# Performance work log

Hardware: AMD Instinct MI355X
Metric: run time of the kernel (lower is better)

The kernel has to match this reference:

```python
import jax, jax.numpy as jnp
import numpy as np

OMEGA_ENC = 0.01   # Encoder.omega
OMEGA_K = 0.1      # KernelMLP.omega
N0, E0 = 4096, 16384     # level-0 graph
N1, E1 = 1024, 8192      # level-1 (pooled) graph
F_IN, H, LAT, DIM = 8, 64, 32, 3
F = H + DIM              # conv input features (x || pos)


def _glorot(key, shape):
    s = jnp.sqrt(2.0 / (shape[0] + shape[-1]))
    return (jax.random.normal(key, shape) * s).astype(jnp.float32)


def setup_inputs() -> dict:
    key = jax.random.key(0)
    ks = jax.random.split(key, 24)
    inp = {
        "x": jax.random.normal(ks[0], (N0, F_IN), jnp.float32),
        "pos": jax.random.normal(ks[1], (N0, DIM), jnp.float32),
        "edge_index": jax.random.randint(ks[2], (2, E0), 0, N0),
        "pool_edge_index1": jax.random.randint(ks[3], (2, E1), 0, N1),
        "pool_pos1": jax.random.normal(ks[4], (N1, DIM), jnp.float32),
        "pool_keep_idx0": jnp.sort(jax.random.randint(ks[5], (N1,), 0, N0)),
        "lin0_w": _glorot(ks[6], (F_IN, H)),
        "lin0_b": 0.01 * jax.random.normal(ks[7], (H,), jnp.float32),
        "lin1_w": _glorot(ks[8], (H, LAT)),
        "lin1_b": 0.01 * jax.random.normal(ks[9], (LAT,), jnp.float32),
    }
    k = 10
    for i in range(2):
        inp[f"conv{i}_k_w0"] = _glorot(ks[k], (DIM + 1, H))
        inp[f"conv{i}_k_b0"] = 0.01 * jax.random.normal(ks[k + 1], (H,), jnp.float32)
        inp[f"conv{i}_k_w1"] = _glorot(ks[k + 2], (H, H))
        inp[f"conv{i}_k_b1"] = 0.01 * jax.random.normal(ks[k + 3], (H,), jnp.float32)
        inp[f"conv{i}_k_w2"] = _glorot(ks[k + 4], (H, F))
        inp[f"conv{i}_k_b2"] = 0.01 * jax.random.normal(ks[k + 5], (F,), jnp.float32)
        inp[f"conv{i}_bias"] = jnp.zeros((H,), jnp.float32)  # zeros() init in torch
        k += 6
    return inp


def _with_self_loops(ei, n):
    # add_remaining_self_loops: input edges are assumed self-loop-free
    loops = jnp.arange(n, dtype=ei.dtype)
    return jnp.concatenate([ei, jnp.stack([loops, loops])], axis=1)


def _kernel_conv(xf, ei, pos, n, w0, b0, w1, b1, w2, b2, bias):
    src, dst = ei[0], ei[1]
    rel = pos[dst] - pos[src]                               # [E,3]
    zero = jnp.all(rel == 0.0, axis=1)                      # self loops -> rho=0, nan phi in torch
    rel_s = jnp.where(zero[:, None], 1.0, rel)              # safe values (avoid nan grads)
    rho = jnp.sqrt(jnp.sum(rel_s * rel_s, axis=1))
    theta = jnp.arctan2(rel_s[:, 1], rel_s[:, 0])
    phi = jnp.arcsin(jnp.clip(rel_s[:, 2] / rho, -1.0, 1.0))
    # torch sets theta/phi to 0 where phi is nan (rho==0); rho itself is 0 there
    rho = jnp.where(zero, 0.0, rho)
    theta = jnp.where(zero, 0.0, theta)
    phi = jnp.where(zero, 0.0, phi)
    feats = jnp.stack([rho, theta / jnp.pi, phi / jnp.pi], axis=1)   # [E,3]
    # KernelMLP lin0 on (feats || channel_id), evaluated for all out channels at once
    base = feats @ w0[:DIM] + b0                            # [E,H]
    ch = jnp.arange(H, dtype=xf.dtype)                      # out_channels == H
    h0 = jnp.sin(OMEGA_K * (base[None] + ch[:, None, None] * w0[DIM][None, None]))  # [C,E,H]
    h1 = jnp.sin(OMEGA_K * (jnp.einsum('ceh,hk->cek', h0, w1) + b1))                # [C,E,H]
    x_j = xf[src]                                           # [E,F]
    # msg[e,c] = (lin2(h1[c,e]) * x_j[e]).sum(); lin2 folded into the contraction
    msg = jnp.einsum('ceh,hf,ef->ec', h1, w2, x_j) + (x_j @ b2)[:, None]            # [E,C]
    return jax.ops.segment_sum(msg, dst, num_segments=n) + bias


def reference(x, edge_index, pos, pool_edge_index1, pool_pos1, pool_keep_idx0,
              lin0_w, lin0_b, lin1_w, lin1_b,
              conv0_k_w0, conv0_k_b0, conv0_k_w1, conv0_k_b1, conv0_k_w2, conv0_k_b2, conv0_bias,
              conv1_k_w0, conv1_k_b0, conv1_k_w1, conv1_k_b1, conv1_k_w2, conv1_k_b2, conv1_bias):
    n0 = x.shape[0]
    h = jnp.sin(OMEGA_ENC * (x @ lin0_w + lin0_b))
    ei0 = _with_self_loops(edge_index, n0)
    h = jnp.sin(OMEGA_ENC * _kernel_conv(jnp.concatenate([h, pos], 1), ei0, pos, n0,
                                         conv0_k_w0, conv0_k_b0, conv0_k_w1, conv0_k_b1,
                                         conv0_k_w2, conv0_k_b2, conv0_bias))
    # max_pool_neighbor_x: per-node max over neighbors incl. self (self loops in ei0)
    h = jax.ops.segment_max(h[ei0[0]], ei0[1], num_segments=n0)[pool_keep_idx0]
    n1 = pool_pos1.shape[0]
    ei1 = _with_self_loops(pool_edge_index1, n1)
    h = jnp.sin(OMEGA_ENC * _kernel_conv(jnp.concatenate([h, pool_pos1], 1), ei1, pool_pos1, n1,
                                         conv1_k_w0, conv1_k_b0, conv1_k_w1, conv1_k_b1,
                                         conv1_k_w2, conv1_k_b2, conv1_bias))
    return jnp.sin(OMEGA_ENC * (h @ lin1_w + lin1_b))   # [N1, LAT]
```

## Files before the change

### kernel.cpp

```cpp
#include <hip/hip_runtime.h>
#include <hip/hip_fp16.h>

#define N0C 4096
#define E0C 16384
#define N1C 1024
#define E1C 8192
#define HC 64
#define FINC 8
#define LATC 32
#define FC 67
#define E0T (E0C + N0C)
#define E1T (E1C + N1C)

typedef float f32x4 __attribute__((ext_vector_type(4)));
typedef _Float16 f16x8 __attribute__((ext_vector_type(8)));

__global__ __launch_bounds__(256) void k_prep(
    const float* __restrict__ x, const float* __restrict__ l0w,
    const float* __restrict__ l0b, const float* __restrict__ posp,
    const float* __restrict__ c0w2, const float* __restrict__ c0b2,
    const float* __restrict__ c0w0, const float* __restrict__ c1w0,
    const float* __restrict__ c0w1, const float* __restrict__ c1w1,
    _Float16* __restrict__ bC0, _Float16* __restrict__ bS0,
    _Float16* __restrict__ bC1, _Float16* __restrict__ bS1,
    _Float16* __restrict__ w1f0, _Float16* __restrict__ w1f1,
    float* __restrict__ tN, float* __restrict__ dN) {
  if (blockIdx.x < 256) {
    __shared__ float w2s[64][69];
    __shared__ float xr[4][64];
    const int tid = threadIdx.x;
    const int wave = __builtin_amdgcn_readfirstlane(tid >> 6), lane = tid & 63;
    for (int idx = tid; idx < HC * FC; idx += 256)
      w2s[idx / FC][idx % FC] = c0w2[idx];
    __syncthreads();
#pragma unroll
    for (int i = 0; i < 4; ++i) {
      const int n = (blockIdx.x * 4 + wave) + i * 1024;
      float a = l0b[lane];
#pragma unroll
      for (int f = 0; f < FINC; ++f) a = fmaf(x[n * FINC + f], l0w[f * HC + lane], a);
      xr[wave][lane] = sinf(0.01f * a);
      __builtin_amdgcn_wave_barrier();
      const float px = posp[n * 3], py = posp[n * 3 + 1], pz = posp[n * 3 + 2];
      float tl = 0.f, ds = 0.f;
#pragma unroll 8
      for (int f = 0; f < HC; ++f) {
        float xv = xr[wave][f];
        tl = fmaf(xv, w2s[lane][f], tl);
        ds = fmaf(xv, c0b2[f], ds);
      }
      tl = fmaf(px, w2s[lane][64], fmaf(py, w2s[lane][65], fmaf(pz, w2s[lane][66], tl)));
      ds = fmaf(px, c0b2[64], fmaf(py, c0b2[65], fmaf(pz, c0b2[66], ds)));
      tN[n * HC + lane] = tl;
      if (lane == 0) dN[n] = ds;
      __builtin_amdgcn_wave_barrier();
    }
  } else {
    int id = (blockIdx.x - 256) * 256 + threadIdx.x;
    if (id < 8192) {
      int lvl = id >> 12, r = id & 4095;
      int fi = r >> 9, lane = (r >> 3) & 63, j = r & 7;
      int nt = fi & 3, ks = fi >> 2;
      int c = nt * 16 + (lane & 15);
      int h = ks * 32 + (lane >> 4) * 8 + j;
      const float* w = lvl ? c1w0 : c0w0;
      float s, cv;
      sincosf(0.1f * (float)c * w[3 * HC + h], &s, &cv);
      (lvl ? bC1 : bC0)[r] = (_Float16)cv;
      (lvl ? bS1 : bS0)[r] = (_Float16)s;
    } else {
      int r0 = id - 8192;
      int lvl = r0 >> 12, r = r0 & 4095;
      int fi = r >> 9, lane = (r >> 3) & 63, j = r & 7;
      int ms = fi & 3, ks = fi >> 2;
      int h = ks * 32 + (lane >> 4) * 8 + j;
      int kout = ms * 16 + (lane & 15);
      const float* w = lvl ? c1w1 : c0w1;
      (lvl ? w1f1 : w1f0)[r] = (_Float16)(0.1f * w[h * HC + kout]);
    }
  }
}

__global__ __launch_bounds__(256, 3) void k_conv(
    const int* __restrict__ ei, int E, int eTot,
    const float* __restrict__ posp,
    const float* __restrict__ tN, const float* __restrict__ dN,
    const float* __restrict__ kw0, const float* __restrict__ kb0,
    const _Float16* __restrict__ bC, const _Float16* __restrict__ bS,
    const _Float16* __restrict__ w1f, const float* __restrict__ b1,
    float* __restrict__ acc_out) {
  __shared__ __attribute__((aligned(16))) _Float16 bCs[4096], bSs[4096];
  __shared__ __attribute__((aligned(16))) _Float16 scS[4][2][64], scC[4][2][64];
  const int tid = threadIdx.x;
  const int wave = __builtin_amdgcn_readfirstlane(tid >> 6), lane = tid & 63;
  const int q = lane >> 4;
  for (int idx = tid; idx < 512; idx += 256) {
    ((f16x8*)bCs)[idx] = ((const f16x8*)bC)[idx];
    ((f16x8*)bSs)[idx] = ((const f16x8*)bS)[idx];
  }
  f16x8 w1r[8];
#pragma unroll
  for (int f = 0; f < 8; ++f) w1r[f] = *(const f16x8*)(w1f + ((f << 6) + lane) * 8);
  f32x4 bbq[4];
#pragma unroll
  for (int ms = 0; ms < 4; ++ms) {
    f32x4 t = *(const f32x4*)(b1 + ms * 16 + q * 4);
    bbq[ms] = t * 0.1f;
  }
  const float kb0v = kb0[lane];
  const float kw0x = kw0[lane], kw0y = kw0[HC + lane], kw0z = kw0[2 * HC + lane];
  __syncthreads();

  const int nW = gridDim.x * 4;
  int e = blockIdx.x * 4 + wave;
  if (e >= eTot) return;

  auto stg = [&](int ee, int& sN, int& dTo, float& sv, float& cv, float& dv) {
    int s, d2;
    if (ee < E) { s = ei[ee]; d2 = ei[E + ee]; } else { s = ee - E; d2 = s; }
    sN = s;
    dTo = d2;
    const float px = posp[s * 3], py = posp[s * 3 + 1], pz = posp[s * 3 + 2];
    const float rx = posp[d2 * 3] - px;
    const float ry = posp[d2 * 3 + 1] - py;
    const float rz = posp[d2 * 3 + 2] - pz;
    float f0 = 0.f, f1 = 0.f, f2 = 0.f;
    if (!(rx == 0.f && ry == 0.f && rz == 0.f)) {
      const float PI_F = 3.14159265358979323846f;
      float rho = sqrtf(rx * rx + ry * ry + rz * rz);
      float th = atan2f(ry, rx);
      float ratio = fminf(1.f, fmaxf(-1.f, rz / rho));
      float ph = asinf(ratio);
      f0 = rho; f1 = th / PI_F; f2 = ph / PI_F;
    }
    float base = fmaf(f0, kw0x, fmaf(f1, kw0y, fmaf(f2, kw0z, kb0v)));
    __sincosf(0.1f * base, &sv, &cv);
    dv = dN[s];
  };

  int s0, d0;
  float sv0, cv0, dv0;
  stg(e, s0, d0, sv0, cv0, dv0);
  int buf = 0;
  scS[wave][0][lane] = (_Float16)sv0;
  scC[wave][0][lane] = (_Float16)cv0;
  __builtin_amdgcn_wave_barrier();

  while (true) {
    const int en = e + nW;
    const bool more = en < eTot;
    f32x4 tr[4];
    {
      const float* trp = tN + (size_t)s0 * HC;
#pragma unroll
      for (int ms = 0; ms < 4; ++ms) tr[ms] = *(const f32x4*)(trp + ms * 16 + q * 4);
    }
    int s1 = 0, d1 = 0;
    float sv1 = 0.f, cv1 = 0.f, dv1 = 0.f;
    if (more) {
      stg(en, s1, d1, sv1, cv1, dv1);
      scS[wave][buf ^ 1][lane] = (_Float16)sv1;
      scC[wave][buf ^ 1][lane] = (_Float16)cv1;
    }
    __builtin_amdgcn_wave_barrier();

    f32x4 acc[4][4];
#pragma unroll
    for (int ms = 0; ms < 4; ++ms)
#pragma unroll
      for (int nt = 0; nt < 4; ++nt) acc[ms][nt] = bbq[ms];
#pragma unroll
    for (int ks = 0; ks < 2; ++ks) {
      f16x8 sv8 = *(const f16x8*)&scS[wave][buf][ks * 32 + q * 8];
      f16x8 cv8 = *(const f16x8*)&scC[wave][buf][ks * 32 + q * 8];
      f16x8 bf[4];
#pragma unroll
      for (int nt = 0; nt < 4; ++nt) {
        f16x8 cb = *(const f16x8*)&bCs[((ks * 4 + nt) * 64 + lane) * 8];
        f16x8 sb = *(const f16x8*)&bSs[((ks * 4 + nt) * 64 + lane) * 8];
        bf[nt] = sv8 * cb + cv8 * sb;
      }
#pragma unroll
      for (int ms = 0; ms < 4; ++ms)
#pragma unroll
        for (int nt = 0; nt < 4; ++nt)
          acc[ms][nt] = __builtin_amdgcn_mfma_f32_16x16x32_f16(
              w1r[ks * 4 + ms], bf[nt], acc[ms][nt], 0, 0, 0);
    }

    float snt0 = 0.f, snt1 = 0.f, snt2 = 0.f, snt3 = 0.f;
#pragma unroll
    for (int ms = 0; ms < 4; ++ms) {
#pragma unroll
      for (int r = 0; r < 4; ++r) {
        float tt = tr[ms][r];
        snt0 = fmaf(__sinf(acc[ms][0][r]), tt, snt0);
        snt1 = fmaf(__sinf(acc[ms][1][r]), tt, snt1);
        snt2 = fmaf(__sinf(acc[ms][2][r]), tt, snt2);
        snt3 = fmaf(__sinf(acc[ms][3][r]), tt, snt3);
      }
    }
    snt0 += __shfl_xor(snt0, 16, 64); snt0 += __shfl_xor(snt0, 32, 64);
    snt1 += __shfl_xor(snt1, 16, 64); snt1 += __shfl_xor(snt1, 32, 64);
    snt2 += __shfl_xor(snt2, 16, 64); snt2 += __shfl_xor(snt2, 32, 64);
    snt3 += __shfl_xor(snt3, 16, 64); snt3 += __shfl_xor(snt3, 32, 64);
    float val = (q == 0) ? snt0 : (q == 1) ? snt1 : (q == 2) ? snt2 : snt3;
    atomicAdd(acc_out + (size_t)d0 * HC + lane, val + dv0);

    if (!more) break;
    e = en; s0 = s1; d0 = d1; dv0 = dv1; buf ^= 1;
  }
}

__global__ __launch_bounds__(256) void k_pool(
    const int* __restrict__ ei, const float* __restrict__ acc0,
    const float* __restrict__ bias, unsigned int* __restrict__ pooled) {
  const int wave = threadIdx.x >> 6, lane = threadIdx.x & 63;
  const int e = blockIdx.x * 4 + wave;
  int s, d;
  if (e < E0C) { s = ei[e]; d = ei[E0C + e]; } else { s = e - E0C; d = s; }
  float v = sinf(0.01f * (acc0[(size_t)s * HC + lane] + bias[lane]));
  unsigned int b = __float_as_uint(v);
  unsigned int key = (b & 0x80000000u) ? ~b : (b | 0x80000000u);
  atomicMax(pooled + (size_t)d * HC + lane, key);
}

__global__ __launch_bounds__(256) void k_t1(
    const unsigned int* __restrict__ pooled, const int* __restrict__ keep,
    const float* __restrict__ ppos, const float* __restrict__ c1w2,
    const float* __restrict__ c1b2, float* __restrict__ tN, float* __restrict__ dN) {
  __shared__ float w2s[64][69];
  __shared__ float xr[4][64];
  const int tid = threadIdx.x;
  const int wave = __builtin_amdgcn_readfirstlane(tid >> 6), lane = tid & 63;
  for (int idx = tid; idx < HC * FC; idx += 256)
    w2s[idx / FC][idx % FC] = c1w2[idx];
  const int i = blockIdx.x * 4 + wave;
  const int n = keep[i];
  unsigned int key = pooled[(size_t)n * HC + lane];
  unsigned int b = (key & 0x80000000u) ? (key & 0x7FFFFFFFu) : ~key;
  xr[wave][lane] = __uint_as_float(b);
  __syncthreads();
  const float px = ppos[i * 3], py = ppos[i * 3 + 1], pz = ppos[i * 3 + 2];
  float tl = 0.f, ds = 0.f;
#pragma unroll 8
  for (int f = 0; f < HC; ++f) {
    float xv = xr[wave][f];
    tl = fmaf(xv, w2s[lane][f], tl);
    ds = fmaf(xv, c1b2[f], ds);
  }
  tl = fmaf(px, w2s[lane][64], fmaf(py, w2s[lane][65], fmaf(pz, w2s[lane][66], tl)));
  ds = fmaf(px, c1b2[64], fmaf(py, c1b2[65], fmaf(pz, c1b2[66], ds)));
  tN[i * HC + lane] = tl;
  if (lane == 0) dN[i] = ds;
}

__global__ __launch_bounds__(256) void k_final(
    const float* __restrict__ acc1, const float* __restrict__ bias,
    const float* __restrict__ l1w, const float* __restrict__ l1b,
    float* __restrict__ outp) {
  __shared__ float hr[4][64];
  const int wave = threadIdx.x >> 6, lane = threadIdx.x & 63;
  const int node = blockIdx.x * 4 + wave;
  hr[wave][lane] = sinf(0.01f * (acc1[(size_t)node * HC + lane] + bias[lane]));
  __syncthreads();
  if (lane < LATC) {
    const float* h = hr[wave];
    float o = l1b[lane];
#pragma unroll 8
    for (int c = 0; c < HC; ++c) o = fmaf(h[c], l1w[c * LATC + lane], o);
    outp[node * LATC + lane] = sinf(0.01f * o);
  }
}

extern "C" void kernel_launch(void* const* d_in, const int* in_sizes, int n_in,
                              void* d_out, int out_size, void* d_ws, size_t ws_size,
                              hipStream_t stream) {
  (void)in_sizes; (void)n_in; (void)out_size; (void)ws_size;
  const float* x    = (const float*)d_in[0];
  const float* pos  = (const float*)d_in[1];
  const int*   ei   = (const int*)d_in[2];
  const int*   pei  = (const int*)d_in[3];
  const float* ppos = (const float*)d_in[4];
  const int*   keep = (const int*)d_in[5];
  const float* l0w  = (const float*)d_in[6];
  const float* l0b  = (const float*)d_in[7];
  const float* l1w  = (const float*)d_in[8];
  const float* l1b  = (const float*)d_in[9];
  const float* c0w0 = (const float*)d_in[10];
  const float* c0b0 = (const float*)d_in[11];
  const float* c0w1 = (const float*)d_in[12];
  const float* c0b1 = (const float*)d_in[13];
  const float* c0w2 = (const float*)d_in[14];
  const float* c0b2 = (const float*)d_in[15];
  const float* c0bias = (const float*)d_in[16];
  const float* c1w0 = (const float*)d_in[17];
  const float* c1b0 = (const float*)d_in[18];
  const float* c1w1 = (const float*)d_in[19];
  const float* c1b1 = (const float*)d_in[20];
  const float* c1w2 = (const float*)d_in[21];
  const float* c1b2 = (const float*)d_in[22];
  const float* c1bias = (const float*)d_in[23];
  float* outp = (float*)d_out;

  char* p = (char*)d_ws;
  auto carve = [&](size_t bytes) -> char* {
    char* r = p;
    p += (bytes + 255) & ~(size_t)255;
    return r;
  };
  float* tN0  = (float*)carve((size_t)N0C * HC * 4);
  float* dN0  = (float*)carve((size_t)N0C * 4);
  float* tN1  = (float*)carve((size_t)N1C * HC * 4);
  float* dN1  = (float*)carve((size_t)N1C * 4);
  _Float16* bC0  = (_Float16*)carve(4096 * 2);
  _Float16* bS0  = (_Float16*)carve(4096 * 2);
  _Float16* bC1  = (_Float16*)carve(4096 * 2);
  _Float16* bS1  = (_Float16*)carve(4096 * 2);
  _Float16* w1f0 = (_Float16*)carve(4096 * 2);
  _Float16* w1f1 = (_Float16*)carve(4096 * 2);
  float* acc0 = (float*)carve((size_t)N0C * HC * 4);
  unsigned int* pooled = (unsigned int*)carve((size_t)N0C * HC * 4);
  float* acc1 = (float*)carve((size_t)N1C * HC * 4);

  hipMemsetAsync(acc0, 0, (size_t)(N0C + N0C + N1C) * HC * 4, stream);

  k_prep<<<256 + 64, 256, 0, stream>>>(x, l0w, l0b, pos, c0w2, c0b2,
                                       c0w0, c1w0, c0w1, c1w1,
                                       bC0, bS0, bC1, bS1, w1f0, w1f1,
                                       tN0, dN0);
  k_conv<<<1536, 256, 0, stream>>>(ei, E0C, E0T, pos, tN0, dN0, c0w0, c0b0,
                                   bC0, bS0, w1f0, c0b1, acc0);
  k_pool<<<E0T / 4, 256, 0, stream>>>(ei, acc0, c0bias, pooled);
  k_t1<<<N1C / 4, 256, 0, stream>>>(pooled, keep, ppos, c1w2, c1b2, tN1, dN1);
  k_conv<<<768, 256, 0, stream>>>(pei, E1C, E1T, ppos, tN1, dN1, c1w0, c1b0,
                                  bC1, bS1, w1f1, c1b1, acc1);
  k_final<<<N1C / 4, 256, 0, stream>>>(acc1, c1bias, l1w, l1b, outp);
}
```

Baseline: 167.2 us.

## Fuse all stages into one persistent kernel with atomic grid barriers

```diff
diff --git a/kernel.cpp b/kernel.cpp
--- a/kernel.cpp
+++ b/kernel.cpp
@@ -11,27 +11,188 @@
 #define FC 67
 #define E0T (E0C + N0C)
 #define E1T (E1C + N1C)
+#define GBLK 512
 
 typedef float f32x4 __attribute__((ext_vector_type(4)));
 typedef _Float16 f16x8 __attribute__((ext_vector_type(8)));
 
-__global__ __launch_bounds__(256) void k_prep(
-    const float* __restrict__ x, const float* __restrict__ l0w,
-    const float* __restrict__ l0b, const float* __restrict__ posp,
+union SharedU {
+  struct { float w2s[64][69]; float xr[4][64]; } prep;
+  struct {
+    _Float16 bCs[4096], bSs[4096];
+    _Float16 scS[4][2][64], scC[4][2][64];
+  } conv;
+};
+
+__device__ __forceinline__ void gsync(unsigned* bar, unsigned target) {
+  __syncthreads();
+  if (threadIdx.x == 0) {
+    __hip_atomic_fetch_add(bar, 1u, __ATOMIC_RELEASE, __HIP_MEMORY_SCOPE_AGENT);
+    while (__hip_atomic_load(bar, __ATOMIC_ACQUIRE, __HIP_MEMORY_SCOPE_AGENT) < target)
+      __builtin_amdgcn_s_sleep(1);
+  }
+  __syncthreads();
+}
+
+__device__ __forceinline__ void conv_phase(
+    SharedU& sh, const int* __restrict__ ei, int E, int eTot,
+    const float* __restrict__ posp, const float* __restrict__ tN,
+    const float* __restrict__ dN, const float* __restrict__ kw0,
+    const float* __restrict__ kb0, const _Float16* __restrict__ bC,
+    const _Float16* __restrict__ bS, const _Float16* __restrict__ w1f,
+    const float* __restrict__ b1, float* __restrict__ acc_out) {
+  const int tid = threadIdx.x;
+  const int wave = __builtin_amdgcn_readfirstlane(tid >> 6), lane = tid & 63;
+  const int q = lane >> 4;
+  auto& cs = sh.conv;
+  for (int idx = tid; idx < 512; idx += 256) {
+    ((f16x8*)cs.bCs)[idx] = ((const f16x8*)bC)[idx];
+    ((f16x8*)cs.bSs)[idx] = ((const f16x8*)bS)[idx];
+  }
+  f16x8 w1r[8];
+#pragma unroll
+  for (int f = 0; f < 8; ++f) w1r[f] = *(const f16x8*)(w1f + ((f << 6) + lane) * 8);
+  f32x4 bbq[4];
+#pragma unroll
+  for (int ms = 0; ms < 4; ++ms) {
+    f32x4 t = *(const f32x4*)(b1 + ms * 16 + q * 4);
+    bbq[ms] = t * 0.1f;
+  }
+  const float kb0v = kb0[lane];
+  const float kw0x = kw0[lane], kw0y = kw0[HC + lane], kw0z = kw0[2 * HC + lane];
+  __syncthreads();
+
+  const int nW = gridDim.x * 4;
+  int e = blockIdx.x * 4 + wave;
+  if (e < eTot) {
+    auto stg = [&](int ee, int& sN, int& dTo, float& sv, float& cv, float& dv) {
+      int s, d2;
+      if (ee < E) { s = ei[ee]; d2 = ei[E + ee]; } else { s = ee - E; d2 = s; }
+      sN = s;
+      dTo = d2;
+      const float px = posp[s * 3], py = posp[s * 3 + 1], pz = posp[s * 3 + 2];
+      const float rx = posp[d2 * 3] - px;
+      const float ry = posp[d2 * 3 + 1] - py;
+      const float rz = posp[d2 * 3 + 2] - pz;
+      float f0 = 0.f, f1 = 0.f, f2 = 0.f;
+      if (!(rx == 0.f && ry == 0.f && rz == 0.f)) {
+        const float PI_F = 3.14159265358979323846f;
+        float rho = sqrtf(rx * rx + ry * ry + rz * rz);
+        float th = atan2f(ry, rx);
+        float ratio = fminf(1.f, fmaxf(-1.f, rz / rho));
+        float ph = asinf(ratio);
+        f0 = rho; f1 = th / PI_F; f2 = ph / PI_F;
+      }
+      float base = fmaf(f0, kw0x, fmaf(f1, kw0y, fmaf(f2, kw0z, kb0v)));
+      __sincosf(0.1f * base, &sv, &cv);
+      dv = dN[s];
+    };
+
+    int s0, d0;
+    float sv0, cv0, dv0;
+    stg(e, s0, d0, sv0, cv0, dv0);
+    int buf = 0;
+    cs.scS[wave][0][lane] = (_Float16)sv0;
+    cs.scC[wave][0][lane] = (_Float16)cv0;
+    __builtin_amdgcn_wave_barrier();
+
+    while (true) {
+      const int en = e + nW;
+      const bool more = en < eTot;
+      f32x4 tr[4];
+      {
+        const float* trp = tN + (size_t)s0 * HC;
+#pragma unroll
+        for (int ms = 0; ms < 4; ++ms) tr[ms] = *(const f32x4*)(trp + ms * 16 + q * 4);
+      }
+      int s1 = 0, d1 = 0;
+      float sv1 = 0.f, cv1 = 0.f, dv1 = 0.f;
+      if (more) {
+        stg(en, s1, d1, sv1, cv1, dv1);
+        cs.scS[wave][buf ^ 1][lane] = (_Float16)sv1;
+        cs.scC[wave][buf ^ 1][lane] = (_Float16)cv1;
+      }
+      __builtin_amdgcn_wave_barrier();
+
+      f32x4 acc[4][4];
+#pragma unroll
+      for (int ms = 0; ms < 4; ++ms)
+#pragma unroll
+        for (int nt = 0; nt < 4; ++nt) acc[ms][nt] = bbq[ms];
+#pragma unroll
+      for (int ks = 0; ks < 2; ++ks) {
+        f16x8 sv8 = *(const f16x8*)&cs.scS[wave][buf][ks * 32 + q * 8];
+        f16x8 cv8 = *(const f16x8*)&cs.scC[wave][buf][ks * 32 + q * 8];
+        f16x8 bf[4];
+#pragma unroll
+        for (int nt = 0; nt < 4; ++nt) {
+          f16x8 cb = *(const f16x8*)&cs.bCs[((ks * 4 + nt) * 64 + lane) * 8];
+          f16x8 sb = *(const f16x8*)&cs.bSs[((ks * 4 + nt) * 64 + lane) * 8];
+          bf[nt] = sv8 * cb + cv8 * sb;
+        }
+#pragma unroll
+        for (int ms = 0; ms < 4; ++ms)
+#pragma unroll
+          for (int nt = 0; nt < 4; ++nt)
+            acc[ms][nt] = __builtin_amdgcn_mfma_f32_16x16x32_f16(
+                w1r[ks * 4 + ms], bf[nt], acc[ms][nt], 0, 0, 0);
+      }
+
+      float snt0 = 0.f, snt1 = 0.f, snt2 = 0.f, snt3 = 0.f;
+#pragma unroll
+      for (int ms = 0; ms < 4; ++ms) {
+#pragma unroll
+        for (int r = 0; r < 4; ++r) {
+          float tt = tr[ms][r];
+          snt0 = fmaf(__sinf(acc[ms][0][r]), tt, snt0);
+          snt1 = fmaf(__sinf(acc[ms][1][r]), tt, snt1);
+          snt2 = fmaf(__sinf(acc[ms][2][r]), tt, snt2);
+          snt3 = fmaf(__sinf(acc[ms][3][r]), tt, snt3);
+        }
+      }
+      snt0 += __shfl_xor(snt0, 16, 64); snt0 += __shfl_xor(snt0, 32, 64);
+      snt1 += __shfl_xor(snt1, 16, 64); snt1 += __shfl_xor(snt1, 32, 64);
+      snt2 += __shfl_xor(snt2, 16, 64); snt2 += __shfl_xor(snt2, 32, 64);
+      snt3 += __shfl_xor(snt3, 16, 64); snt3 += __shfl_xor(snt3, 32, 64);
+      float val = (q == 0) ? snt0 : (q == 1) ? snt1 : (q == 2) ? snt2 : snt3;
+      atomicAdd(acc_out + (size_t)d0 * HC + lane, val + dv0);
+
+      if (!more) break;
+      e = en; s0 = s1; d0 = d1; dv0 = dv1; buf ^= 1;
+    }
+  }
+}
+
+__global__ __launch_bounds__(256, 3) void k_mega(
+    const float* __restrict__ x, const float* __restrict__ posp,
+    const int* __restrict__ ei, const int* __restrict__ pei,
+    const float* __restrict__ ppos, const int* __restrict__ keep,
+    const float* __restrict__ l0w, const float* __restrict__ l0b,
+    const float* __restrict__ l1w, const float* __restrict__ l1b,
+    const float* __restrict__ c0w0, const float* __restrict__ c0b0,
+    const float* __restrict__ c0w1, const float* __restrict__ c0b1,
     const float* __restrict__ c0w2, const float* __restrict__ c0b2,
-    const float* __restrict__ c0w0, const float* __restrict__ c1w0,
-    const float* __restrict__ c0w1, const float* __restrict__ c1w1,
+    const float* __restrict__ c0bias,
+    const float* __restrict__ c1w0, const float* __restrict__ c1b0,
+    const float* __restrict__ c1w1, const float* __restrict__ c1b1,
+    const float* __restrict__ c1w2, const float* __restrict__ c1b2,
+    const float* __restrict__ c1bias,
+    float* __restrict__ tN0, float* __restrict__ dN0,
+    float* __restrict__ tN1, float* __restrict__ dN1,
     _Float16* __restrict__ bC0, _Float16* __restrict__ bS0,
     _Float16* __restrict__ bC1, _Float16* __restrict__ bS1,
     _Float16* __restrict__ w1f0, _Float16* __restrict__ w1f1,
-    float* __restrict__ tN, float* __restrict__ dN) {
+    float* __restrict__ acc0, unsigned* __restrict__ pooled,
+    float* __restrict__ acc1, unsigned* __restrict__ bar,
+    float* __restrict__ outp) {
+  __shared__ SharedU sh;
+  const int tid = threadIdx.x;
+  const int wave = __builtin_amdgcn_readfirstlane(tid >> 6), lane = tid & 63;
+  const unsigned G = gridDim.x;
+
   if (blockIdx.x < 256) {
-    __shared__ float w2s[64][69];
-    __shared__ float xr[4][64];
-    const int tid = threadIdx.x;
-    const int wave = __builtin_amdgcn_readfirstlane(tid >> 6), lane = tid & 63;
     for (int idx = tid; idx < HC * FC; idx += 256)
-      w2s[idx / FC][idx % FC] = c0w2[idx];
+      sh.prep.w2s[idx / FC][idx % FC] = c0w2[idx];
     __syncthreads();
 #pragma unroll
     for (int i = 0; i < 4; ++i) {
@@ -39,30 +200,31 @@
       float a = l0b[lane];
 #pragma unroll
       for (int f = 0; f < FINC; ++f) a = fmaf(x[n * FINC + f], l0w[f * HC + lane], a);
-      xr[wave][lane] = sinf(0.01f * a);
+      sh.prep.xr[wave][lane] = sinf(0.01f * a);
       __builtin_amdgcn_wave_barrier();
       const float px = posp[n * 3], py = posp[n * 3 + 1], pz = posp[n * 3 + 2];
       float tl = 0.f, ds = 0.f;
 #pragma unroll 8
       for (int f = 0; f < HC; ++f) {
-        float xv = xr[wave][f];
-        tl = fmaf(xv, w2s[lane][f], tl);
+        float xv = sh.prep.xr[wave][f];
+        tl = fmaf(xv, sh.prep.w2s[lane][f], tl);
         ds = fmaf(xv, c0b2[f], ds);
       }
-      tl = fmaf(px, w2s[lane][64], fmaf(py, w2s[lane][65], fmaf(pz, w2s[lane][66], tl)));
+      tl = fmaf(px, sh.prep.w2s[lane][64],
+           fmaf(py, sh.prep.w2s[lane][65], fmaf(pz, sh.prep.w2s[lane][66], tl)));
       ds = fmaf(px, c0b2[64], fmaf(py, c0b2[65], fmaf(pz, c0b2[66], ds)));
-      tN[n * HC + lane] = tl;
-      if (lane == 0) dN[n] = ds;
+      tN0[n * HC + lane] = tl;
+      if (lane == 0) dN0[n] = ds;
       __builtin_amdgcn_wave_barrier();
     }
-  } else {
-    int id = (blockIdx.x - 256) * 256 + threadIdx.x;
+  } else if (blockIdx.x < 320) {
+    int id = (blockIdx.x - 256) * 256 + tid;
     if (id < 8192) {
       int lvl = id >> 12, r = id & 4095;
-      int fi = r >> 9, lane = (r >> 3) & 63, j = r & 7;
+      int fi = r >> 9, ln = (r >> 3) & 63, j = r & 7;
       int nt = fi & 3, ks = fi >> 2;
-      int c = nt * 16 + (lane & 15);
-      int h = ks * 32 + (lane >> 4) * 8 + j;
+      int c = nt * 16 + (ln & 15);
+      int h = ks * 32 + (ln >> 4) * 8 + j;
       const float* w = lvl ? c1w0 : c0w0;
       float s, cv;
       sincosf(0.1f * (float)c * w[3 * HC + h], &s, &cv);
@@ -71,205 +233,80 @@
     } else {
       int r0 = id - 8192;
       int lvl = r0 >> 12, r = r0 & 4095;
-      int fi = r >> 9, lane = (r >> 3) & 63, j = r & 7;
+      int fi = r >> 9, ln = (r >> 3) & 63, j = r & 7;
       int ms = fi & 3, ks = fi >> 2;
-      int h = ks * 32 + (lane >> 4) * 8 + j;
-      int kout = ms * 16 + (lane & 15);
+      int h = ks * 32 + (ln >> 4) * 8 + j;
+      int kout = ms * 16 + (ln & 15);
       const float* w = lvl ? c1w1 : c0w1;
       (lvl ? w1f1 : w1f0)[r] = (_Float16)(0.1f * w[h * HC + kout]);
     }
-  }
-}
-
-__global__ __launch_bounds__(256, 3) void k_conv(
-    const int* __restrict__ ei, int E, int eTot,
-    const float* __restrict__ posp,
-    const float* __restrict__ tN, const float* __restrict__ dN,
-    const float* __restrict__ kw0, const float* __restrict__ kb0,
-    const _Float16* __restrict__ bC, const _Float16* __restrict__ bS,
-    const _Float16* __restrict__ w1f, const float* __restrict__ b1,
-    float* __restrict__ acc_out) {
-  __shared__ __attribute__((aligned(16))) _Float16 bCs[4096], bSs[4096];
-  __shared__ __attribute__((aligned(16))) _Float16 scS[4][2][64], scC[4][2][64];
-  const int tid = threadIdx.x;
-  const int wave = __builtin_amdgcn_readfirstlane(tid >> 6), lane = tid & 63;
-  const int q = lane >> 4;
-  for (int idx = tid; idx < 512; idx += 256) {
-    ((f16x8*)bCs)[idx] = ((const f16x8*)bC)[idx];
-    ((f16x8*)bSs)[idx] = ((const f16x8*)bS)[idx];
-  }
-  f16x8 w1r[8];
-#pragma unroll
-  for (int f = 0; f < 8; ++f) w1r[f] = *(const f16x8*)(w1f + ((f << 6) + lane) * 8);
-  f32x4 bbq[4];
-#pragma unroll
-  for (int ms = 0; ms < 4; ++ms) {
-    f32x4 t = *(const f32x4*)(b1 + ms * 16 + q * 4);
-    bbq[ms] = t * 0.1f;
-  }
-  const float kb0v = kb0[lane];
-  const float kw0x = kw0[lane], kw0y = kw0[HC + lane], kw0z = kw0[2 * HC + lane];
-  __syncthreads();
-
-  const int nW = gridDim.x * 4;
-  int e = blockIdx.x * 4 + wave;
-  if (e >= eTot) return;
-
-  auto stg = [&](int ee, int& sN, int& dTo, float& sv, float& cv, float& dv) {
-    int s, d2;
-    if (ee < E) { s = ei[ee]; d2 = ei[E + ee]; } else { s = ee - E; d2 = s; }
-    sN = s;
-    dTo = d2;
-    const float px = posp[s * 3], py = posp[s * 3 + 1], pz = posp[s * 3 + 2];
-    const float rx = posp[d2 * 3] - px;
-    const float ry = posp[d2 * 3 + 1] - py;
-    const float rz = posp[d2 * 3 + 2] - pz;
-    float f0 = 0.f, f1 = 0.f, f2 = 0.f;
-    if (!(rx == 0.f && ry == 0.f && rz == 0.f)) {
-      const float PI_F = 3.14159265358979323846f;
-      float rho = sqrtf(rx * rx + ry * ry + rz * rz);
-      float th = atan2f(ry, rx);
-      float ratio = fminf(1.f, fmaxf(-1.f, rz / rho));
-      float ph = asinf(ratio);
-      f0 = rho; f1 = th / PI_F; f2 = ph / PI_F;
-    }
-    float base = fmaf(f0, kw0x, fmaf(f1, kw0y, fmaf(f2, kw0z, kb0v)));
-    __sincosf(0.1f * base, &sv, &cv);
-    dv = dN[s];
-  };
-
-  int s0, d0;
-  float sv0, cv0, dv0;
-  stg(e, s0, d0, sv0, cv0, dv0);
-  int buf = 0;
-  scS[wave][0][lane] = (_Float16)sv0;
-  scC[wave][0][lane] = (_Float16)cv0;
-  __builtin_amdgcn_wave_barrier();
-
-  while (true) {
-    const int en = e + nW;
-    const bool more = en < eTot;
-    f32x4 tr[4];
-    {
-      const float* trp = tN + (size_t)s0 * HC;
-#pragma unroll
-      for (int ms = 0; ms < 4; ++ms) tr[ms] = *(const f32x4*)(trp + ms * 16 + q * 4);
-    }
-    int s1 = 0, d1 = 0;
-    float sv1 = 0.f, cv1 = 0.f, dv1 = 0.f;
-    if (more) {
-      stg(en, s1, d1, sv1, cv1, dv1);
-      scS[wave][buf ^ 1][lane] = (_Float16)sv1;
-      scC[wave][buf ^ 1][lane] = (_Float16)cv1;
-    }
-    __builtin_amdgcn_wave_barrier();
-
-    f32x4 acc[4][4];
-#pragma unroll
-    for (int ms = 0; ms < 4; ++ms)
-#pragma unroll
-      for (int nt = 0; nt < 4; ++nt) acc[ms][nt] = bbq[ms];
-#pragma unroll
-    for (int ks = 0; ks < 2; ++ks) {
-      f16x8 sv8 = *(const f16x8*)&scS[wave][buf][ks * 32 + q * 8];
-      f16x8 cv8 = *(const f16x8*)&scC[wave][buf][ks * 32 + q * 8];
-      f16x8 bf[4];
-#pragma unroll
-      for (int nt = 0; nt < 4; ++nt) {
-        f16x8 cb = *(const f16x8*)&bCs[((ks * 4 + nt) * 64 + lane) * 8];
-        f16x8 sb = *(const f16x8*)&bSs[((ks * 4 + nt) * 64 + lane) * 8];
-        bf[nt] = sv8 * cb + cv8 * sb;
-      }
-#pragma unroll
-      for (int ms = 0; ms < 4; ++ms)
-#pragma unroll
-        for (int nt = 0; nt < 4; ++nt)
-          acc[ms][nt] = __builtin_amdgcn_mfma_f32_16x16x32_f16(
-              w1r[ks * 4 + ms], bf[nt], acc[ms][nt], 0, 0, 0);
-    }
-
-    float snt0 = 0.f, snt1 = 0.f, snt2 = 0.f, snt3 = 0.f;
-#pragma unroll
-    for (int ms = 0; ms < 4; ++ms) {
-#pragma unroll
-      for (int r = 0; r < 4; ++r) {
-        float tt = tr[ms][r];
-        snt0 = fmaf(__sinf(acc[ms][0][r]), tt, snt0);
-        snt1 = fmaf(__sinf(acc[ms][1][r]), tt, snt1);
-        snt2 = fmaf(__sinf(acc[ms][2][r]), tt, snt2);
-        snt3 = fmaf(__sinf(acc[ms][3][r]), tt, snt3);
-      }
-    }
-    snt0 += __shfl_xor(snt0, 16, 64); snt0 += __shfl_xor(snt0, 32, 64);
-    snt1 += __shfl_xor(snt1, 16, 64); snt1 += __shfl_xor(snt1, 32, 64);
-    snt2 += __shfl_xor(snt2, 16, 64); snt2 += __shfl_xor(snt2, 32, 64);
-    snt3 += __shfl_xor(snt3, 16, 64); snt3 += __shfl_xor(snt3, 32, 64);
-    float val = (q == 0) ? snt0 : (q == 1) ? snt1 : (q == 2) ? snt2 : snt3;
-    atomicAdd(acc_out + (size_t)d0 * HC + lane, val + dv0);
-
-    if (!more) break;
-    e = en; s0 = s1; d0 = d1; dv0 = dv1; buf ^= 1;
-  }
-}
-
-__global__ __launch_bounds__(256) void k_pool(
-    const int* __restrict__ ei, const float* __restrict__ acc0,
-    const float* __restrict__ bias, unsigned int* __restrict__ pooled) {
-  const int wave = threadIdx.x >> 6, lane = threadIdx.x & 63;
-  const int e = blockIdx.x * 4 + wave;
-  int s, d;
-  if (e < E0C) { s = ei[e]; d = ei[E0C + e]; } else { s = e - E0C; d = s; }
-  float v = sinf(0.01f * (acc0[(size_t)s * HC + lane] + bias[lane]));
-  unsigned int b = __float_as_uint(v);
-  unsigned int key = (b & 0x80000000u) ? ~b : (b | 0x80000000u);
-  atomicMax(pooled + (size_t)d * HC + lane, key);
-}
-
-__global__ __launch_bounds__(256) void k_t1(
-    const unsigned int* __restrict__ pooled, const int* __restrict__ keep,
-    const float* __restrict__ ppos, const float* __restrict__ c1w2,
-    const float* __restrict__ c1b2, float* __restrict__ tN, float* __restrict__ dN) {
-  __shared__ float w2s[64][69];
-  __shared__ float xr[4][64];
-  const int tid = threadIdx.x;
-  const int wave = __builtin_amdgcn_readfirstlane(tid >> 6), lane = tid & 63;
-  for (int idx = tid; idx < HC * FC; idx += 256)
-    w2s[idx / FC][idx % FC] = c1w2[idx];
-  const int i = blockIdx.x * 4 + wave;
-  const int n = keep[i];
-  unsigned int key = pooled[(size_t)n * HC + lane];
-  unsigned int b = (key & 0x80000000u) ? (key & 0x7FFFFFFFu) : ~key;
-  xr[wave][lane] = __uint_as_float(b);
-  __syncthreads();
-  const float px = ppos[i * 3], py = ppos[i * 3 + 1], pz = ppos[i * 3 + 2];
-  float tl = 0.f, ds = 0.f;
+  } else {
+    int t = (blockIdx.x - 320) * 256 + tid;
+    f32x4 z = {0.f, 0.f, 0.f, 0.f};
+    f32x4* zp = (f32x4*)acc0;
+    zp[t] = z;
+    zp[t + 49152] = z;
+    zp[t + 98304] = z;
+  }
+  gsync(bar, G * 1);
+
+  conv_phase(sh, ei, E0C, E0T, posp, tN0, dN0, c0w0, c0b0, bC0, bS0, w1f0,
+             c0b1, acc0);
+  gsync(bar, G * 2);
+
+  {
+    const float bz = c0bias[lane];
+    for (int e = blockIdx.x * 4 + wave; e < E0T; e += gridDim.x * 4) {
+      int s, d;
+      if (e < E0C) { s = ei[e]; d = ei[E0C + e]; } else { s = e - E0C; d = s; }
+      float v = sinf(0.01f * (acc0[(size_t)s * HC + lane] + bz));
+      unsigned b = __float_as_uint(v);
+      unsigned key = (b & 0x80000000u) ? ~b : (b | 0x80000000u);
+      atomicMax(pooled + (size_t)d * HC + lane, key);
+    }
+  }
+  gsync(bar, G * 3);
+
+  if (blockIdx.x < 256) {
+    for (int idx = tid; idx < HC * FC; idx += 256)
+      sh.prep.w2s[idx / FC][idx % FC] = c1w2[idx];
+    const int i = blockIdx.x * 4 + wave;
+    const int n = keep[i];
+    unsigned key = pooled[(size_t)n * HC + lane];
+    unsigned b = (key & 0x80000000u) ? (key & 0x7FFFFFFFu) : ~key;
+    sh.prep.xr[wave][lane] = __uint_as_float(b);
+    __syncthreads();
+    const float px = ppos[i * 3], py = ppos[i * 3 + 1], pz = ppos[i * 3 + 2];
+    float tl = 0.f, ds = 0.f;
 #pragma unroll 8
-  for (int f = 0; f < HC; ++f) {
-    float xv = xr[wave][f];
-    tl = fmaf(xv, w2s[lane][f], tl);
-    ds = fmaf(xv, c1b2[f], ds);
-  }
-  tl = fmaf(px, w2s[lane][64], fmaf(py, w2s[lane][65], fmaf(pz, w2s[lane][66], tl)));
-  ds = fmaf(px, c1b2[64], fmaf(py, c1b2[65], fmaf(pz, c1b2[66], ds)));
-  tN[i * HC + lane] = tl;
-  if (lane == 0) dN[i] = ds;
-}
-
-__global__ __launch_bounds__(256) void k_final(
-    const float* __restrict__ acc1, const float* __restrict__ bias,
-    const float* __restrict__ l1w, const float* __restrict__ l1b,
-    float* __restrict__ outp) {
-  __shared__ float hr[4][64];
-  const int wave = threadIdx.x >> 6, lane = threadIdx.x & 63;
-  const int node = blockIdx.x * 4 + wave;
-  hr[wave][lane] = sinf(0.01f * (acc1[(size_t)node * HC + lane] + bias[lane]));
-  __syncthreads();
-  if (lane < LATC) {
-    const float* h = hr[wave];
-    float o = l1b[lane];
+    for (int f = 0; f < HC; ++f) {
+      float xv = sh.prep.xr[wave][f];
+      tl = fmaf(xv, sh.prep.w2s[lane][f], tl);
+      ds = fmaf(xv, c1b2[f], ds);
+    }
+    tl = fmaf(px, sh.prep.w2s[lane][64],
+         fmaf(py, sh.prep.w2s[lane][65], fmaf(pz, sh.prep.w2s[lane][66], tl)));
+    ds = fmaf(px, c1b2[64], fmaf(py, c1b2[65], fmaf(pz, c1b2[66], ds)));
+    tN1[i * HC + lane] = tl;
+    if (lane == 0) dN1[i] = ds;
+  }
+  gsync(bar, G * 4);
+
+  conv_phase(sh, pei, E1C, E1T, ppos, tN1, dN1, c1w0, c1b0, bC1, bS1, w1f1,
+             c1b1, acc1);
+  gsync(bar, G * 5);
+
+  if (blockIdx.x < 256) {
+    const int node = blockIdx.x * 4 + wave;
+    sh.prep.xr[wave][lane] = sinf(0.01f * (acc1[(size_t)node * HC + lane] + c1bias[lane]));
+    __syncthreads();
+    if (lane < LATC) {
+      const float* h = sh.prep.xr[wave];
+      float o = l1b[lane];
 #pragma unroll 8
-    for (int c = 0; c < HC; ++c) o = fmaf(h[c], l1w[c * LATC + lane], o);
-    outp[node * LATC + lane] = sinf(0.01f * o);
+      for (int c = 0; c < HC; ++c) o = fmaf(h[c], l1w[c * LATC + lane], o);
+      outp[node * LATC + lane] = sinf(0.01f * o);
+    }
   }
 }
 
@@ -320,20 +357,16 @@
   _Float16* w1f0 = (_Float16*)carve(4096 * 2);
   _Float16* w1f1 = (_Float16*)carve(4096 * 2);
   float* acc0 = (float*)carve((size_t)N0C * HC * 4);
-  unsigned int* pooled = (unsigned int*)carve((size_t)N0C * HC * 4);
+  unsigned* pooled = (unsigned*)carve((size_t)N0C * HC * 4);
   float* acc1 = (float*)carve((size_t)N1C * HC * 4);
-
-  hipMemsetAsync(acc0, 0, (size_t)(N0C + N0C + N1C) * HC * 4, stream);
-
-  k_prep<<<256 + 64, 256, 0, stream>>>(x, l0w, l0b, pos, c0w2, c0b2,
-                                       c0w0, c1w0, c0w1, c1w1,
-                                       bC0, bS0, bC1, bS1, w1f0, w1f1,
-                                       tN0, dN0);
-  k_conv<<<1536, 256, 0, stream>>>(ei, E0C, E0T, pos, tN0, dN0, c0w0, c0b0,
-                                   bC0, bS0, w1f0, c0b1, acc0);
-  k_pool<<<E0T / 4, 256, 0, stream>>>(ei, acc0, c0bias, pooled);
-  k_t1<<<N1C / 4, 256, 0, stream>>>(pooled, keep, ppos, c1w2, c1b2, tN1, dN1);
-  k_conv<<<768, 256, 0, stream>>>(pei, E1C, E1T, ppos, tN1, dN1, c1w0, c1b0,
-                                  bC1, bS1, w1f1, c1b1, acc1);
-  k_final<<<N1C / 4, 256, 0, stream>>>(acc1, c1bias, l1w, l1b, outp);
+  unsigned* bar = (unsigned*)carve(256);
+
+  hipMemsetAsync(bar, 0, 256, stream);
+
+  k_mega<<<GBLK, 256, 0, stream>>>(
+      x, pos, ei, pei, ppos, keep, l0w, l0b, l1w, l1b,
+      c0w0, c0b0, c0w1, c0b1, c0w2, c0b2, c0bias,
+      c1w0, c1b0, c1w1, c1b1, c1w2, c1b2, c1bias,
+      tN0, dN0, tN1, dN1, bC0, bS0, bC1, bS1, w1f0, w1f1,
+      acc0, pooled, acc1, bar, outp);
 }
```

After: 397.1 us. +137.6%, slower.
